# Performance work log

Measured on AMD Instinct MI355X. Metric: run time of the kernel, lower is better.

The kernel has to match this reference:

```python
import jax, jax.numpy as jnp
import numpy as np

N, E, B = 50000, 800000, 512
IN, H, D, C = 128, 4, 64, 1
NG, GH = 200, 256


def gat_layer(h, W, al, ar, src, dst, res_w=None, res_id=False, act=True):
    """DGL-style GATConv: fc -> per-head attn logits -> edge softmax by dst -> scatter-sum."""
    Nn = h.shape[0]
    Hh, Dd = al.shape
    f = (h @ W).reshape(Nn, Hh, Dd)                       # [N,H,D]
    el = jnp.einsum('nhd,hd->nh', f, al)                  # [N,H]
    er = jnp.einsum('nhd,hd->nh', f, ar)
    e = jax.nn.leaky_relu(el[src] + er[dst], 0.2)         # [E,H]
    m = jax.ops.segment_max(e, dst, num_segments=Nn)      # softmax over in-edges of each dst
    ex = jnp.exp(e - m[dst])
    den = jax.ops.segment_sum(ex, dst, num_segments=Nn)
    a = ex / den[dst]                                      # [E,H]
    rst = jax.ops.segment_sum(f[src] * a[..., None], dst, num_segments=Nn)  # [N,H,D]
    if res_id:
        rst = rst + h.reshape(Nn, Hh, Dd)
    elif res_w is not None:
        rst = rst + (h @ res_w).reshape(Nn, Hh, Dd)
    if act:
        rst = jax.nn.elu(rst)
    return rst


def setup_inputs() -> dict:
    key = jax.random.key(0)
    ks = jax.random.split(key, 24)
    s = 0.05
    HD = H * D
    return {
        'feat': jax.random.normal(ks[0], (N, IN), jnp.float32),
        'src': jax.random.randint(ks[1], (E,), 0, N, jnp.int32),
        'dst': jax.random.randint(ks[2], (E,), 0, N, jnp.int32),
        'graph_ids': jnp.sort(jax.random.randint(ks[3], (N,), 0, B, jnp.int32)),
        'g_feat': jax.random.normal(ks[4], (B, NG), jnp.float32),
        'W0': jax.random.normal(ks[5], (IN, HD), jnp.float32) * s,
        'al0': jax.random.normal(ks[6], (H, D), jnp.float32) * s,
        'ar0': jax.random.normal(ks[7], (H, D), jnp.float32) * s,
        'W1': jax.random.normal(ks[8], (HD, HD), jnp.float32) * s,
        'al1': jax.random.normal(ks[9], (H, D), jnp.float32) * s,
        'ar1': jax.random.normal(ks[10], (H, D), jnp.float32) * s,
        'W2': jax.random.normal(ks[11], (HD, HD), jnp.float32) * s,
        'al2': jax.random.normal(ks[12], (H, D), jnp.float32) * s,
        'ar2': jax.random.normal(ks[13], (H, D), jnp.float32) * s,
        'W3': jax.random.normal(ks[14], (HD, H * C), jnp.float32) * s,
        'al3': jax.random.normal(ks[15], (H, C), jnp.float32) * s,
        'ar3': jax.random.normal(ks[16], (H, C), jnp.float32) * s,
        'resW3': jax.random.normal(ks[17], (HD, H * C), jnp.float32) * s,
        'gw1': jax.random.normal(ks[18], (NG, GH), jnp.float32) * s,
        'gb1': jnp.zeros((GH,), jnp.float32),
        'gw2': jax.random.normal(ks[19], (GH, GH), jnp.float32) * s,
        'gb2': jnp.zeros((GH,), jnp.float32),
        'lw': jax.random.normal(ks[20], (H + GH, C), jnp.float32) * s,
        'lb': jnp.zeros((C,), jnp.float32),
    }


def reference(feat, src, dst, graph_ids, g_feat,
              W0, al0, ar0, W1, al1, ar1, W2, al2, ar2,
              W3, al3, ar3, resW3, gw1, gb1, gw2, gb2, lw, lb):
    h = gat_layer(feat, W0, al0, ar0, src, dst).reshape(N, -1)
    h = gat_layer(h, W1, al1, ar1, src, dst, res_id=True).reshape(N, -1)
    h = gat_layer(h, W2, al2, ar2, src, dst, res_id=True).reshape(N, -1)
    hn = gat_layer(h, W3, al3, ar3, src, dst, res_w=resW3, act=False)   # [N,H,C]
    latent = jax.ops.segment_sum(hn, graph_ids, num_segments=B).mean(axis=-1)  # [B,H]
    lg = jax.nn.relu(jax.nn.relu(g_feat @ gw1 + gb1) @ gw2 + gb2)        # [B,GH]
    return jnp.concatenate([latent, lg], axis=1) @ lw + lb               # [B,C]
```

## Files before the change

### kernel.cpp

```cpp
#include <hip/hip_runtime.h>
#include <hip/hip_bf16.h>
#include <math.h>

#define N_NODES 50000
#define N_EDGES 800000
#define NB      512
#define IN_F    128
#define NH      4
#define HD      64
#define HDIM    256
#define NG_F    200
#define GH_F    256
#define CSZ     196

typedef __attribute__((ext_vector_type(8))) short short8;
typedef __attribute__((ext_vector_type(8))) unsigned short u16x8;
typedef __attribute__((ext_vector_type(4))) float f32x4;
typedef __attribute__((ext_vector_type(2))) float f32x2;

static __device__ __forceinline__ float lrelu(float x){ return x > 0.f ? x : 0.2f*x; }
static __device__ __forceinline__ float fexp(float x){ return __expf(x); }

static __device__ __forceinline__ unsigned short f2b(float f){
  union { float f; unsigned int u; } v; v.f = f;
  unsigned int r = v.u + 0x7fffu + ((v.u >> 16) & 1u);
  return (unsigned short)(r >> 16);
}
static __device__ __forceinline__ float b2f(unsigned short b){
  union { unsigned int u; float f; } v; v.u = ((unsigned int)b) << 16;
  return v.f;
}
static __device__ __forceinline__ float u2f(unsigned int u){
  union { unsigned int u; float f; } v; v.u = u;
  return v.f;
}

__global__ __launch_bounds__(256) void k_f2b(const float* __restrict__ in, unsigned short* __restrict__ out, int n4){
  int i = blockIdx.x*256 + threadIdx.x;
  if (i >= n4) return;
  float4 v = ((const float4*)in)[i];
  ushort4 o;
  o.x = f2b(v.x); o.y = f2b(v.y); o.z = f2b(v.z); o.w = f2b(v.w);
  ((ushort4*)out)[i] = o;
}

__global__ __launch_bounds__(256) void k_padg(const float* __restrict__ g, unsigned short* __restrict__ out){
  int idx = blockIdx.x*256 + threadIdx.x;
  if (idx >= NB*256) return;
  int b = idx >> 8, k = idx & 255;
  out[idx] = (k < NG_F) ? f2b(g[b*NG_F + k]) : (unsigned short)0;
}

__global__ __launch_bounds__(256) void k_w2bt(const float* __restrict__ W, unsigned short* __restrict__ Bt,
                                              int Ksrc, int Kdst, int NC){
  __shared__ unsigned short t[32][33];
  int bn = blockIdx.x*32;
  int bk = blockIdx.y*32;
  int lx = threadIdx.x & 31, ly = threadIdx.x >> 5;
  #pragma unroll
  for (int i = 0; i < 32; i += 8) {
    int kr = bk + ly + i;
    t[ly+i][lx] = (kr < Ksrc) ? f2b(W[(size_t)kr*NC + bn+lx]) : (unsigned short)0;
  }
  __syncthreads();
  #pragma unroll
  for (int i = 0; i < 32; i += 8)
    Bt[(size_t)(bn+ly+i)*Kdst + bk+lx] = t[lx][ly+i];
}

__global__ __launch_bounds__(256) void k_hist(const int* __restrict__ dst, int* __restrict__ deg){
  int e = blockIdx.x*256 + threadIdx.x;
  if (e < N_EDGES) atomicAdd(&deg[dst[e]], 1);
}

__global__ __launch_bounds__(64) void k_s1a(const int* __restrict__ deg, int* __restrict__ blocksum){
  int b = blockIdx.x, lane = threadIdx.x;
  int start = b*CSZ, end = min(start+CSZ, N_NODES);
  int s = 0;
  for (int i = start + lane; i < end; i += 64) s += deg[i];
  #pragma unroll
  for (int m = 1; m < 64; m <<= 1) s += __shfl_xor(s, m);
  if (lane == 0) blocksum[b] = s;
}

__global__ __launch_bounds__(256) void k_s1b(const int* __restrict__ blocksum, int* __restrict__ chunkoff){
  __shared__ int sd[256];
  int t = threadIdx.x;
  int own = blocksum[t];
  sd[t] = own; __syncthreads();
  for (int off = 1; off < 256; off <<= 1) {
    int v = (t >= off) ? sd[t-off] : 0;
    __syncthreads();
    sd[t] += v;
    __syncthreads();
  }
  chunkoff[t] = sd[t] - own;
}

__global__ __launch_bounds__(64) void k_scan2(const int* __restrict__ deg, const int* __restrict__ chunkoff,
                                              int* __restrict__ row_start, int* __restrict__ cursor){
  int b = blockIdx.x, lane = threadIdx.x;
  int start = b*CSZ, end = min(start+CSZ, N_NODES);
  int run = chunkoff[b];
  for (int k = start; k < end; k += 64) {
    int idx = k + lane;
    int v = (idx < end) ? deg[idx] : 0;
    int inc = v;
    #pragma unroll
    for (int off = 1; off < 64; off <<= 1) {
      int t = __shfl_up(inc, off);
      if (lane >= off) inc += t;
    }
    int excl = run + inc - v;
    if (idx < end) { row_start[idx] = excl; cursor[idx] = excl; }
    run += __shfl(inc, 63);
  }
  if (b == 255 && lane == 0) row_start[N_NODES] = run;
}

__global__ __launch_bounds__(256) void k_scatter(const int* __restrict__ dst, const int* __restrict__ src,
                                                 int* __restrict__ cursor, int* __restrict__ csrc){
  int e = blockIdx.x*256 + threadIdx.x;
  if (e < N_EDGES) {
    int p = atomicAdd(&cursor[dst[e]], 1);
    csrc[p] = src[e];
  }
}

__global__ __launch_bounds__(256) void k_goff(const int* __restrict__ gid, int* __restrict__ goff){
  int n = blockIdx.x*256 + threadIdx.x;
  if (n >= N_NODES) return;
  int ca = gid[n];
  if (n == 0) {
    for (int g = 0; g <= ca; g++) goff[g] = 0;
  } else {
    int pa = gid[n-1];
    for (int g = pa+1; g <= ca; g++) goff[g] = n;
  }
  if (n == N_NODES-1) {
    for (int g = ca+1; g <= NB; g++) goff[g] = N_NODES;
  }
}

__global__ __launch_bounds__(256) void k_gemm_bf16(const unsigned short* __restrict__ A,
                                                   const unsigned short* __restrict__ Bt,
                                                   unsigned short* __restrict__ C,
                                                   const float* __restrict__ bias, int act,
                                                   const float* __restrict__ al, const float* __restrict__ ar,
                                                   float* __restrict__ el, float* __restrict__ er,
                                                   int M, int K, int NC, int ntiles){
  __shared__ unsigned short As[128][72];
  __shared__ unsigned short Bs[64][72];
  __shared__ float sEL[2][2][4][16];
  __shared__ float sER[2][2][4][16];
  const int bid = blockIdx.x;
  const int xcd = bid & 7;
  const int r   = bid >> 3;
  const int q   = r / ntiles;
  const int nt  = r - q*ntiles;
  const int mtile = q*8 + xcd;
  if (mtile*128 >= M) return;
  const int bm = mtile*128, bn = nt*64;
  const int tid = threadIdx.x;
  const int wid = tid >> 6, lane = tid & 63;
  const int wr = wid >> 1, wc = wid & 1;
  const int l15 = lane & 15, lg = lane >> 4;
  const int ar_ = tid >> 1, ak = (tid & 1) * 32;
  const int br = tid >> 2, bkp = (tid & 3) * 16;
  int agrow = bm + ar_; if (agrow >= M) agrow = M - 1;

  f32x4 acc[4][2] = {};
  for (int k0 = 0; k0 < K; k0 += 64) {
    #pragma unroll
    for (int p = 0; p < 4; p++)
      *(uint4*)(&As[ar_][ak + p*8]) = *(const uint4*)(A + (size_t)agrow*K + k0 + ak + p*8);
    #pragma unroll
    for (int p = 0; p < 2; p++)
      *(uint4*)(&Bs[br][bkp + p*8]) = *(const uint4*)(Bt + (size_t)(bn + br)*K + k0 + bkp + p*8);
    __syncthreads();
    #pragma unroll
    for (int ks = 0; ks < 2; ks++) {
      short8 af[4], bf[2];
      #pragma unroll
      for (int m = 0; m < 4; m++) af[m] = *(const short8*)(&As[wr*64 + m*16 + l15][ks*32 + lg*8]);
      #pragma unroll
      for (int nn = 0; nn < 2; nn++) bf[nn] = *(const short8*)(&Bs[wc*32 + nn*16 + l15][ks*32 + lg*8]);
      #pragma unroll
      for (int m = 0; m < 4; m++)
        #pragma unroll
        for (int nn = 0; nn < 2; nn++)
          acc[m][nn] = __builtin_amdgcn_mfma_f32_16x16x32_bf16(af[m], bf[nn], acc[m][nn], 0, 0, 0);
    }
    __syncthreads();
  }
  #pragma unroll
  for (int m = 0; m < 4; m++)
    #pragma unroll
    for (int nn = 0; nn < 2; nn++) {
      int col = bn + wc*32 + nn*16 + l15;
      float bv = bias ? bias[col] : 0.f;
      #pragma unroll
      for (int i = 0; i < 4; i++) {
        int row = bm + wr*64 + m*16 + lg*4 + i;
        if (row < M) {
          float v = acc[m][nn][i] + bv;
          if (act) v = fmaxf(v, 0.f);
          C[(size_t)row*NC + col] = f2b(v);
        }
      }
    }
  if (al) {
    int hidx = bn >> 6;
    float pl[16], pr[16];
    #pragma unroll
    for (int m = 0; m < 4; m++)
      #pragma unroll
      for (int i = 0; i < 4; i++) {
        float sl = 0.f, sr = 0.f;
        #pragma unroll
        for (int nn = 0; nn < 2; nn++) {
          int colh = wc*32 + nn*16 + l15;
          sl += acc[m][nn][i] * al[hidx*64 + colh];
          sr += acc[m][nn][i] * ar[hidx*64 + colh];
        }
        pl[m*4+i] = sl; pr[m*4+i] = sr;
      }
    #pragma unroll
    for (int k = 0; k < 16; k++) {
      #pragma unroll
      for (int mm = 1; mm < 16; mm <<= 1) {
        pl[k] += __shfl_xor(pl[k], mm);
        pr[k] += __shfl_xor(pr[k], mm);
      }
    }
    if (l15 == 0) {
      #pragma unroll
      for (int k = 0; k < 16; k++) { sEL[wr][wc][lg][k] = pl[k]; sER[wr][wc][lg][k] = pr[k]; }
    }
    __syncthreads();
    if (tid < 128) {
      int k = tid & 15;
      int lg2 = (tid >> 4) & 3;
      int wr2 = tid >> 6;
      float vl = sEL[wr2][0][lg2][k] + sEL[wr2][1][lg2][k];
      float vr = sER[wr2][0][lg2][k] + sER[wr2][1][lg2][k];
      int m = k >> 2, i = k & 3;
      int row = bm + wr2*64 + m*16 + lg2*4 + i;
      if (row < M) { el[row*NH + hidx] = vl; er[row*NH + hidx] = vr; }
    }
  }
}

__global__ __launch_bounds__(256) void k_agg(
    const unsigned short* __restrict__ f, const float* __restrict__ el, const float* __restrict__ er,
    const int* __restrict__ row_start, const int* __restrict__ csrc,
    const unsigned short* __restrict__ resid, unsigned short* __restrict__ out, int act){
  __shared__ float sA[4][64][4];
  __shared__ int   sS[4][64];
  int wid  = threadIdx.x >> 6;
  int lane = threadIdx.x & 63;
  int n = blockIdx.x*4 + wid;
  int half = lane >> 5;
  int c    = lane & 31;
  int h    = c >> 3;
  int e0 = row_start[n], e1 = row_start[n+1];
  float4 erv = ((const float4*)er)[n];

  float4 den = make_float4(0.f,0.f,0.f,0.f);
  f32x2 acc2[4] = {};

  for (int base = e0; base < e1; base += 64) {
    int cnt = min(64, e1 - base);
    int   s_l = 0;
    float4 a4 = make_float4(0.f,0.f,0.f,0.f);
    if (base + lane < e1) {
      s_l = csrc[base + lane];
      float4 ev = ((const float4*)el)[s_l];
      a4.x = fexp(lrelu(ev.x + erv.x));
      a4.y = fexp(lrelu(ev.y + erv.y));
      a4.z = fexp(lrelu(ev.z + erv.z));
      a4.w = fexp(lrelu(ev.w + erv.w));
    }
    den.x += a4.x; den.y += a4.y; den.z += a4.z; den.w += a4.w;
    sS[wid][lane] = s_l;
    sA[wid][lane][0] = a4.x; sA[wid][lane][1] = a4.y;
    sA[wid][lane][2] = a4.z; sA[wid][lane][3] = a4.w;
    __builtin_amdgcn_sched_barrier(0);
    for (int j = 0; j < cnt; j += 8) {
      uint4 u[4]; f32x2 aa[4];
      #pragma unroll
      for (int p = 0; p < 4; p++) {
        int jj = j + 2*p + half;
        float a = 0.f; int s;
        if (jj < cnt) { s = sS[wid][jj]; a = sA[wid][jj][h]; } else { s = sS[wid][j]; }
        u[p] = *(const uint4*)(f + (size_t)s*HDIM + c*8);
        aa[p][0] = a; aa[p][1] = a;
      }
      #pragma unroll
      for (int p = 0; p < 4; p++) {
        f32x2 p0, p1, p2, p3;
        p0[0] = u2f(u[p].x << 16); p0[1] = u2f(u[p].x & 0xffff0000u);
        p1[0] = u2f(u[p].y << 16); p1[1] = u2f(u[p].y & 0xffff0000u);
        p2[0] = u2f(u[p].z << 16); p2[1] = u2f(u[p].z & 0xffff0000u);
        p3[0] = u2f(u[p].w << 16); p3[1] = u2f(u[p].w & 0xffff0000u);
        asm volatile("v_pk_fma_f32 %0, %1, %2, %0" : "+v"(acc2[0]) : "v"(p0), "v"(aa[p]));
        asm volatile("v_pk_fma_f32 %0, %1, %2, %0" : "+v"(acc2[1]) : "v"(p1), "v"(aa[p]));
        asm volatile("v_pk_fma_f32 %0, %1, %2, %0" : "+v"(acc2[2]) : "v"(p2), "v"(aa[p]));
        asm volatile("v_pk_fma_f32 %0, %1, %2, %0" : "+v"(acc2[3]) : "v"(p3), "v"(aa[p]));
      }
    }
  }
  #pragma unroll
  for (int m = 1; m < 64; m <<= 1) {
    den.x += __shfl_xor(den.x, m);
    den.y += __shfl_xor(den.y, m);
    den.z += __shfl_xor(den.z, m);
    den.w += __shfl_xor(den.w, m);
  }
  float accv[8];
  #pragma unroll
  for (int q = 0; q < 4; q++) {
    accv[2*q]   = acc2[q][0] + __shfl_xor(acc2[q][0], 32);
    accv[2*q+1] = acc2[q][1] + __shfl_xor(acc2[q][1], 32);
  }

  float d_h = h==0 ? den.x : h==1 ? den.y : h==2 ? den.z : den.w;
  float inv = d_h > 0.f ? 1.0f/d_h : 0.f;

  if (half == 0) {
    #pragma unroll
    for (int k = 0; k < 8; k++) accv[k] *= inv;
    if (resid) {
      u16x8 r = *(const u16x8*)(resid + (size_t)n*HDIM + c*8);
      #pragma unroll
      for (int k = 0; k < 8; k++) accv[k] += b2f((unsigned short)r[k]);
    }
    if (act) {
      #pragma unroll
      for (int k = 0; k < 8; k++) accv[k] = accv[k] > 0.f ? accv[k] : (fexp(accv[k]) - 1.0f);
    }
    u16x8 o;
    #pragma unroll
    for (int k = 0; k < 8; k++) o[k] = f2b(accv[k]);
    *(u16x8*)(out + (size_t)n*HDIM + c*8) = o;
  }
}

__global__ __launch_bounds__(256) void k_l3proj(const unsigned short* __restrict__ h,
    const float* __restrict__ W3, const float* __restrict__ rW3,
    const float* __restrict__ al3, const float* __restrict__ ar3,
    float* __restrict__ f3, float* __restrict__ r3,
    float* __restrict__ el3, float* __restrict__ er3){
  int n = blockIdx.x*4 + (threadIdx.x >> 6);
  int lane = threadIdx.x & 63;
  if (n >= N_NODES) return;
  ushort4 u = ((const ushort4*)(h + (size_t)n*HDIM))[lane];
  float hk[4] = {b2f(u.x), b2f(u.y), b2f(u.z), b2f(u.w)};
  const float4* w  = (const float4*)W3;
  const float4* rw = (const float4*)rW3;
  float4 acc = make_float4(0.f,0.f,0.f,0.f);
  float4 rac = make_float4(0.f,0.f,0.f,0.f);
  #pragma unroll
  for (int j = 0; j < 4; j++) {
    float4 wv = w[lane*4 + j];
    float4 rv = rw[lane*4 + j];
    acc.x += hk[j]*wv.x; acc.y += hk[j]*wv.y; acc.z += hk[j]*wv.z; acc.w += hk[j]*wv.w;
    rac.x += hk[j]*rv.x; rac.y += hk[j]*rv.y; rac.z += hk[j]*rv.z; rac.w += hk[j]*rv.w;
  }
  #pragma unroll
  for (int m = 1; m < 64; m <<= 1) {
    acc.x += __shfl_xor(acc.x, m); acc.y += __shfl_xor(acc.y, m);
    acc.z += __shfl_xor(acc.z, m); acc.w += __shfl_xor(acc.w, m);
    rac.x += __shfl_xor(rac.x, m); rac.y += __shfl_xor(rac.y, m);
    rac.z += __shfl_xor(rac.z, m); rac.w += __shfl_xor(rac.w, m);
  }
  if (lane == 0) {
    ((float4*)f3)[n] = acc;
    ((float4*)r3)[n] = rac;
    float4 e1 = make_float4(acc.x*al3[0], acc.y*al3[1], acc.z*al3[2], acc.w*al3[3]);
    float4 e2 = make_float4(acc.x*ar3[0], acc.y*ar3[1], acc.z*ar3[2], acc.w*ar3[3]);
    ((float4*)el3)[n] = e1;
    ((float4*)er3)[n] = e2;
  }
}

__global__ __launch_bounds__(256) void k_l3node(
    const float* __restrict__ f3, const float* __restrict__ el3, const float* __restrict__ er3,
    const int* __restrict__ row_start, const int* __restrict__ csrc,
    const float* __restrict__ r3, float* __restrict__ hn){
  int g = threadIdx.x >> 4;
  int l = threadIdx.x & 15;
  int n = blockIdx.x*16 + g;
  int e0 = row_start[n], e1 = row_start[n+1];
  float4 erv = ((const float4*)er3)[n];

  float4 dn  = make_float4(0.f,0.f,0.f,0.f);
  float4 acc = make_float4(0.f,0.f,0.f,0.f);
  for (int i = e0 + l; i < e1; i += 16) {
    int s = csrc[i];
    float4 ev = ((const float4*)el3)[s];
    float ax = fexp(lrelu(ev.x + erv.x));
    float ay = fexp(lrelu(ev.y + erv.y));
    float az = fexp(lrelu(ev.z + erv.z));
    float aw = fexp(lrelu(ev.w + erv.w));
    dn.x += ax; dn.y += ay; dn.z += az; dn.w += aw;
    float4 fv = ((const float4*)f3)[s];
    acc.x += ax*fv.x; acc.y += ay*fv.y; acc.z += az*fv.z; acc.w += aw*fv.w;
  }
  #pragma unroll
  for (int m = 1; m < 16; m <<= 1) {
    dn.x += __shfl_xor(dn.x, m);  dn.y += __shfl_xor(dn.y, m);
    dn.z += __shfl_xor(dn.z, m);  dn.w += __shfl_xor(dn.w, m);
    acc.x += __shfl_xor(acc.x, m); acc.y += __shfl_xor(acc.y, m);
    acc.z += __shfl_xor(acc.z, m); acc.w += __shfl_xor(acc.w, m);
  }
  if (l == 0) {
    float4 rv = ((const float4*)r3)[n];
    float4 o;
    o.x = (dn.x > 0.f ? acc.x/dn.x : 0.f) + rv.x;
    o.y = (dn.y > 0.f ? acc.y/dn.y : 0.f) + rv.y;
    o.z = (dn.z > 0.f ? acc.z/dn.z : 0.f) + rv.z;
    o.w = (dn.w > 0.f ? acc.w/dn.w : 0.f) + rv.w;
    ((float4*)hn)[n] = o;
  }
}

__global__ __launch_bounds__(64) void k_gseg(const float* __restrict__ hn, const int* __restrict__ goff,
                                             float* __restrict__ latent){
  int b = blockIdx.x;
  int lane = threadIdx.x;
  int n0 = goff[b], n1 = goff[b+1];
  float4 s = make_float4(0.f,0.f,0.f,0.f);
  for (int n = n0 + lane; n < n1; n += 64) {
    float4 v = ((const float4*)hn)[n];
    s.x += v.x; s.y += v.y; s.z += v.z; s.w += v.w;
  }
  #pragma unroll
  for (int m = 1; m < 64; m <<= 1) {
    s.x += __shfl_xor(s.x, m); s.y += __shfl_xor(s.y, m);
    s.z += __shfl_xor(s.z, m); s.w += __shfl_xor(s.w, m);
  }
  if (lane == 0) ((float4*)latent)[b] = s;
}

__global__ __launch_bounds__(256) void k_final(const float* __restrict__ latent, const unsigned short* __restrict__ lgb,
    const float* __restrict__ lw, const float* __restrict__ lb, float* __restrict__ out){
  int b = blockIdx.x*4 + (threadIdx.x >> 6);
  int lane = threadIdx.x & 63;
  if (b >= NB) return;
  ushort4 u = ((const ushort4*)(lgb + (size_t)b*GH_F))[lane];
  float4 wv = ((const float4*)(lw + NH))[lane];
  float s = b2f(u.x)*wv.x + b2f(u.y)*wv.y + b2f(u.z)*wv.z + b2f(u.w)*wv.w;
  #pragma unroll
  for (int m = 1; m < 64; m <<= 1) s += __shfl_xor(s, m);
  if (lane == 0) {
    float4 lv = ((const float4*)latent)[b];
    out[b] = s + lv.x*lw[0] + lv.y*lw[1] + lv.z*lw[2] + lv.w*lw[3] + lb[0];
  }
}

__global__ __launch_bounds__(256) void k_sentinel(float* out){
  int i = blockIdx.x*256 + threadIdx.x;
  if (i < NB) out[i] = -12345.0f;
}

extern "C" void kernel_launch(void* const* d_in, const int* in_sizes, int n_in,
                              void* d_out, int out_size, void* d_ws, size_t ws_size,
                              hipStream_t stream){
  const float* feat   = (const float*)d_in[0];
  const int*   src    = (const int*)d_in[1];
  const int*   dst    = (const int*)d_in[2];
  const int*   gid    = (const int*)d_in[3];
  const float* g_feat = (const float*)d_in[4];
  const float* W0   = (const float*)d_in[5];
  const float* al0  = (const float*)d_in[6];
  const float* ar0  = (const float*)d_in[7];
  const float* W1   = (const float*)d_in[8];
  const float* al1  = (const float*)d_in[9];
  const float* ar1  = (const float*)d_in[10];
  const float* W2   = (const float*)d_in[11];
  const float* al2  = (const float*)d_in[12];
  const float* ar2  = (const float*)d_in[13];
  const float* W3   = (const float*)d_in[14];
  const float* al3  = (const float*)d_in[15];
  const float* ar3  = (const float*)d_in[16];
  const float* rW3  = (const float*)d_in[17];
  const float* gw1  = (const float*)d_in[18];
  const float* gb1  = (const float*)d_in[19];
  const float* gw2  = (const float*)d_in[20];
  const float* gb2  = (const float*)d_in[21];
  const float* lw   = (const float*)d_in[22];
  const float* lb   = (const float*)d_in[23];
  float* out = (float*)d_out;

  char* base = (char*)d_ws;
  size_t off = 0;
  auto alloc = [&](size_t bytes)->char* {
    char* r = base + off;
    off += (bytes + 255) & ~(size_t)255;
    return r;
  };
  unsigned short* featb = (unsigned short*)alloc((size_t)N_NODES*IN_F*2);
  unsigned short* fbuf  = (unsigned short*)alloc((size_t)N_NODES*HDIM*2);
  unsigned short* hA    = (unsigned short*)alloc((size_t)N_NODES*HDIM*2);
  unsigned short* hB    = (unsigned short*)alloc((size_t)N_NODES*HDIM*2);
  unsigned short* W0t   = (unsigned short*)alloc((size_t)IN_F*HDIM*2);
  unsigned short* W1t   = (unsigned short*)alloc((size_t)HDIM*HDIM*2);
  unsigned short* W2t   = (unsigned short*)alloc((size_t)HDIM*HDIM*2);
  unsigned short* gfb   = (unsigned short*)alloc((size_t)NB*256*2);
  unsigned short* gw1t  = (unsigned short*)alloc((size_t)GH_F*256*2);
  unsigned short* gw2t  = (unsigned short*)alloc((size_t)GH_F*GH_F*2);
  unsigned short* g1b   = (unsigned short*)alloc((size_t)NB*GH_F*2);
  unsigned short* lgb   = (unsigned short*)alloc((size_t)NB*GH_F*2);
  float* el   = (float*)alloc((size_t)N_NODES*NH*4);
  float* er   = (float*)alloc((size_t)N_NODES*NH*4);
  float* f3   = (float*)alloc((size_t)N_NODES*NH*4);
  float* r3   = (float*)alloc((size_t)N_NODES*NH*4);
  float* hn   = (float*)alloc((size_t)N_NODES*NH*4);
  int* deg       = (int*)alloc((size_t)N_NODES*4);
  int* row_start = (int*)alloc((size_t)(N_NODES+1)*4);
  int* cursor    = (int*)alloc((size_t)N_NODES*4);
  int* csrc      = (int*)alloc((size_t)N_EDGES*4);
  int* blocksum  = (int*)alloc(256*4);
  int* chunkoff  = (int*)alloc(256*4);
  int* goff      = (int*)alloc((size_t)(NB+1)*4);
  float* latent  = (float*)alloc((size_t)NB*NH*4);

  if (off > ws_size) {
    k_sentinel<<<2, 256, 0, stream>>>(out);
    return;
  }

  k_f2b<<<((N_NODES*IN_F/4)+255)/256, 256, 0, stream>>>(feat, featb, N_NODES*IN_F/4);
  {
    dim3 g0(HDIM/32, IN_F/32), g12(HDIM/32, HDIM/32), gm(256/32, 256/32);
    k_w2bt<<<g0, 256, 0, stream>>>(W0, W0t, IN_F, IN_F, HDIM);
    k_w2bt<<<g12, 256, 0, stream>>>(W1, W1t, HDIM, HDIM, HDIM);
    k_w2bt<<<g12, 256, 0, stream>>>(W2, W2t, HDIM, HDIM, HDIM);
    k_w2bt<<<gm, 256, 0, stream>>>(gw1, gw1t, NG_F, 256, GH_F);
    k_w2bt<<<gm, 256, 0, stream>>>(gw2, gw2t, GH_F, GH_F, GH_F);
  }
  k_padg<<<(NB*256+255)/256, 256, 0, stream>>>(g_feat, gfb);

  hipMemsetAsync(deg, 0, (size_t)N_NODES*4, stream);
  k_hist<<<(N_EDGES+255)/256, 256, 0, stream>>>(dst, deg);
  k_s1a<<<256, 64, 0, stream>>>(deg, blocksum);
  k_s1b<<<1, 256, 0, stream>>>(blocksum, chunkoff);
  k_scan2<<<256, 64, 0, stream>>>(deg, chunkoff, row_start, cursor);
  k_scatter<<<(N_EDGES+255)/256, 256, 0, stream>>>(dst, src, cursor, csrc);
  k_goff<<<(N_NODES+255)/256, 256, 0, stream>>>(gid, goff);

  const int mt_main = (N_NODES + 127) / 128;
  const int grid_main = 8 * ((mt_main + 7) / 8) * 4;
  const int mt_mlp = (NB + 127) / 128;
  const int grid_mlp = 8 * ((mt_mlp + 7) / 8) * 4;

  k_gemm_bf16<<<grid_main, 256, 0, stream>>>(featb, W0t, fbuf, nullptr, 0, al0, ar0, el, er, N_NODES, IN_F, HDIM, 4);
  k_agg<<<N_NODES/4, 256, 0, stream>>>(fbuf, el, er, row_start, csrc, nullptr, hA, 1);

  k_gemm_bf16<<<grid_main, 256, 0, stream>>>(hA, W1t, fbuf, nullptr, 0, al1, ar1, el, er, N_NODES, HDIM, HDIM, 4);
  k_agg<<<N_NODES/4, 256, 0, stream>>>(fbuf, el, er, row_start, csrc, hA, hB, 1);

  k_gemm_bf16<<<grid_main, 256, 0, stream>>>(hB, W2t, fbuf, nullptr, 0, al2, ar2, el, er, N_NODES, HDIM, HDIM, 4);
  k_agg<<<N_NODES/4, 256, 0, stream>>>(fbuf, el, er, row_start, csrc, hB, hA, 1);

  k_l3proj<<<(N_NODES+3)/4, 256, 0, stream>>>(hA, W3, rW3, al3, ar3, f3, r3, el, er);
  k_l3node<<<N_NODES/16, 256, 0, stream>>>(f3, el, er, row_start, csrc, r3, hn);
  k_gseg<<<NB, 64, 0, stream>>>(hn, goff, latent);

  k_gemm_bf16<<<grid_mlp, 256, 0, stream>>>(gfb, gw1t, g1b, gb1, 1, nullptr, nullptr, nullptr, nullptr, NB, 256, GH_F, 4);
  k_gemm_bf16<<<grid_mlp, 256, 0, stream>>>(g1b, gw2t, lgb, gb2, 1, nullptr, nullptr, nullptr, nullptr, NB, GH_F, GH_F, 4);
  k_final<<<(NB+3)/4, 256, 0, stream>>>(latent, lgb, lw, lb, out);
}
```

Measured before the change: 470.7 us.

## Split aggregation feature halves across XCD groups for L2 locality

The aggregation kernel now gives each node two blocks. Each block handles one half of the 256-wide feature row (two heads). The block-to-XCD mapping (bid&7) sends the two halves to separate groups of four XCDs, so each XCD's L2 only caches half of the gathered feature matrix. Inside a block, four lane groups of 16 handle four edges per step instead of two edges across 32 lanes. This adds a second shuffle reduction. The edge-score exp work is also duplicated, since both blocks for a node recompute it.

Result: slower. 490.2 us (+4.2%).

```diff
diff --git a/kernel.cpp b/kernel.cpp
--- a/kernel.cpp
+++ b/kernel.cpp
@@ -257,12 +257,18 @@
     const unsigned short* __restrict__ resid, unsigned short* __restrict__ out, int act){
   __shared__ float sA[4][64][4];
   __shared__ int   sS[4][64];
+  int bid  = blockIdx.x;
+  int xcd  = bid & 7;
+  int half = xcd >> 2;
+  int sub  = xcd & 3;
+  int nblk = (bid >> 3)*4 + sub;
   int wid  = threadIdx.x >> 6;
   int lane = threadIdx.x & 63;
-  int n = blockIdx.x*4 + wid;
-  int half = lane >> 5;
-  int c    = lane & 31;
-  int h    = c >> 3;
+  int n = nblk*4 + wid;
+  int eq = lane >> 4;
+  int fl = lane & 15;
+  int fc = half*16 + fl;
+  int h  = fc >> 3;
   int e0 = row_start[n], e1 = row_start[n+1];
   float4 erv = ((const float4*)er)[n];
 
@@ -286,14 +292,14 @@
     sA[wid][lane][0] = a4.x; sA[wid][lane][1] = a4.y;
     sA[wid][lane][2] = a4.z; sA[wid][lane][3] = a4.w;
     __builtin_amdgcn_sched_barrier(0);
-    for (int j = 0; j < cnt; j += 8) {
+    for (int j = 0; j < cnt; j += 16) {
       uint4 u[4]; f32x2 aa[4];
       #pragma unroll
       for (int p = 0; p < 4; p++) {
-        int jj = j + 2*p + half;
+        int jj = j + 4*p + eq;
         float a = 0.f; int s;
         if (jj < cnt) { s = sS[wid][jj]; a = sA[wid][jj][h]; } else { s = sS[wid][j]; }
-        u[p] = *(const uint4*)(f + (size_t)s*HDIM + c*8);
+        u[p] = *(const uint4*)(f + (size_t)s*HDIM + fc*8);
         aa[p][0] = a; aa[p][1] = a;
       }
       #pragma unroll
@@ -320,18 +326,20 @@
   float accv[8];
   #pragma unroll
   for (int q = 0; q < 4; q++) {
-    accv[2*q]   = acc2[q][0] + __shfl_xor(acc2[q][0], 32);
-    accv[2*q+1] = acc2[q][1] + __shfl_xor(acc2[q][1], 32);
+    float v0 = acc2[q][0], v1 = acc2[q][1];
+    v0 += __shfl_xor(v0, 16); v0 += __shfl_xor(v0, 32);
+    v1 += __shfl_xor(v1, 16); v1 += __shfl_xor(v1, 32);
+    accv[2*q] = v0; accv[2*q+1] = v1;
   }
 
   float d_h = h==0 ? den.x : h==1 ? den.y : h==2 ? den.z : den.w;
   float inv = d_h > 0.f ? 1.0f/d_h : 0.f;
 
-  if (half == 0) {
+  if (eq == 0) {
     #pragma unroll
     for (int k = 0; k < 8; k++) accv[k] *= inv;
     if (resid) {
-      u16x8 r = *(const u16x8*)(resid + (size_t)n*HDIM + c*8);
+      u16x8 r = *(const u16x8*)(resid + (size_t)n*HDIM + fc*8);
       #pragma unroll
       for (int k = 0; k < 8; k++) accv[k] += b2f((unsigned short)r[k]);
     }
@@ -342,7 +350,7 @@
     u16x8 o;
     #pragma unroll
     for (int k = 0; k < 8; k++) o[k] = f2b(accv[k]);
-    *(u16x8*)(out + (size_t)n*HDIM + c*8) = o;
+    *(u16x8*)(out + (size_t)n*HDIM + fc*8) = o;
   }
 }
 
@@ -554,15 +562,16 @@
   const int grid_main = 8 * ((mt_main + 7) / 8) * 4;
   const int mt_mlp = (NB + 127) / 128;
   const int grid_mlp = 8 * ((mt_mlp + 7) / 8) * 4;
+  const int grid_agg = 8 * (N_NODES / 16);
 
   k_gemm_bf16<<<grid_main, 256, 0, stream>>>(featb, W0t, fbuf, nullptr, 0, al0, ar0, el, er, N_NODES, IN_F, HDIM, 4);
-  k_agg<<<N_NODES/4, 256, 0, stream>>>(fbuf, el, er, row_start, csrc, nullptr, hA, 1);
+  k_agg<<<grid_agg, 256, 0, stream>>>(fbuf, el, er, row_start, csrc, nullptr, hA, 1);
 
   k_gemm_bf16<<<grid_main, 256, 0, stream>>>(hA, W1t, fbuf, nullptr, 0, al1, ar1, el, er, N_NODES, HDIM, HDIM, 4);
-  k_agg<<<N_NODES/4, 256, 0, stream>>>(fbuf, el, er, row_start, csrc, hA, hB, 1);
+  k_agg<<<grid_agg, 256, 0, stream>>>(fbuf, el, er, row_start, csrc, hA, hB, 1);
 
   k_gemm_bf16<<<grid_main, 256, 0, stream>>>(hB, W2t, fbuf, nullptr, 0, al2, ar2, el, er, N_NODES, HDIM, HDIM, 4);
-  k_agg<<<N_NODES/4, 256, 0, stream>>>(fbuf, el, er, row_start, csrc, hB, hA, 1);
+  k_agg<<<grid_agg, 256, 0, stream>>>(fbuf, el, er, row_start, csrc, hB, hA, 1);
 
   k_l3proj<<<(N_NODES+3)/4, 256, 0, stream>>>(hA, W3, rW3, al3, ar3, f3, r3, el, er);
   k_l3node<<<N_NODES/16, 256, 0, stream>>>(f3, el, er, row_start, csrc, r3, hn);
```
